# Performance work log

Measured on AMD Instinct MI355X. Metric: run time of the kernel, lower is better.

## Reference

```python
import jax, jax.numpy as jnp
import numpy as np

NEG_SLOPE = 0.2


def _gat_layer(x, W, a_src, a_dst, b, src, dst, heads, out_dim, concat):
    # x: [N, F_in]; W: [F_in, heads*out_dim]; a_src/a_dst: [heads, out_dim]
    N = x.shape[0]
    h = (x @ W).reshape(N, heads, out_dim)              # [N, H, D]
    alpha_src = jnp.sum(h * a_src[None], axis=-1)       # [N, H]
    alpha_dst = jnp.sum(h * a_dst[None], axis=-1)       # [N, H]
    e = jax.nn.leaky_relu(alpha_src[src] + alpha_dst[dst], NEG_SLOPE)  # [E, H]
    # scatter-softmax over incoming edges of each destination node
    e_max = jax.ops.segment_max(e, dst, num_segments=N)            # [N, H]
    e_exp = jnp.exp(e - e_max[dst])                                 # [E, H]
    e_sum = jax.ops.segment_sum(e_exp, dst, num_segments=N)        # [N, H]
    alpha = e_exp / e_sum[dst]                                      # [E, H]
    # weighted scatter-sum of source features
    msg = alpha[:, :, None] * h[src]                                # [E, H, D]
    out = jax.ops.segment_sum(msg, dst, num_segments=N)             # [N, H, D]
    if concat:
        out = out.reshape(N, heads * out_dim)
    else:
        out = out.mean(axis=1)
    return out + b


def setup_inputs() -> dict:
    key = jax.random.key(0)
    ks = jax.random.split(key, 9)
    N, E, F_in, C = 100000, 1600000, 512, 40
    x = jax.random.normal(ks[0], (N, F_in), dtype=jnp.float32)
    edge_index = jax.random.randint(ks[1], (2, E), 0, N, dtype=jnp.int64)
    s = 0.05
    return {
        "x": x,
        "edge_index": edge_index,
        "W1": jax.random.normal(ks[2], (F_in, 64), dtype=jnp.float32) * s,
        "att_src1": jax.random.normal(ks[3], (8, 8), dtype=jnp.float32) * s,
        "att_dst1": jax.random.normal(ks[4], (8, 8), dtype=jnp.float32) * s,
        "b1": jnp.zeros((64,), dtype=jnp.float32),
        "W2": jax.random.normal(ks[5], (64, C), dtype=jnp.float32) * s,
        "att_src2": jax.random.normal(ks[6], (1, C), dtype=jnp.float32) * s,
        "att_dst2": jax.random.normal(ks[7], (1, C), dtype=jnp.float32) * s,
        "b2": jnp.zeros((C,), dtype=jnp.float32),
    }


def reference(x, edge_index, W1, att_src1, att_dst1, b1, W2, att_src2, att_dst2, b2):
    N = x.shape[0]
    # PyG GATConv default add_self_loops=True
    loops = jnp.tile(jnp.arange(N, dtype=edge_index.dtype)[None, :], (2, 1))
    ei = jnp.concatenate([edge_index, loops], axis=1)
    src, dst = ei[0], ei[1]
    # dropout layers are identity at inference
    h = _gat_layer(x, W1, att_src1, att_dst1, b1, src, dst, heads=8, out_dim=8, concat=True)
    h = jax.nn.elu(h)
    out = _gat_layer(h, W2, att_src2, att_dst2, b2, src, dst, heads=1, out_dim=40, concat=True)
    return jax.nn.log_softmax(out, axis=1)
```

## Files before the change

### kernel.cpp

```cpp
#include <hip/hip_runtime.h>
#include <hip/hip_bf16.h>

typedef __bf16 bf16x8 __attribute__((ext_vector_type(8)));
typedef float f32x4 __attribute__((ext_vector_type(4)));
typedef unsigned u32x2 __attribute__((ext_vector_type(2)));
typedef unsigned u32x4 __attribute__((ext_vector_type(4)));

#define LR_SLOPE 0.2f
#define NBKMAX 256
#define BCAP   12288

static __device__ __forceinline__ unsigned short f2bf(float f){
  union { float f; unsigned u; } v; v.f = f;
  unsigned u = v.u;
  u += 0x7fffu + ((u >> 16) & 1u);
  return (unsigned short)(u >> 16);
}
static __device__ __forceinline__ float bf2f(unsigned short us){
  union { unsigned u; float f; } v; v.u = ((unsigned)us) << 16;
  return v.f;
}
static __device__ __forceinline__ unsigned pk2(float a, float b){
  return (unsigned)f2bf(a) | ((unsigned)f2bf(b) << 16);
}
static __device__ __forceinline__ unsigned char f2e4m3(float f){
  return (unsigned char)(__builtin_amdgcn_cvt_pk_fp8_f32(f, 0.f, 0, false) & 0xff);
}
static __device__ __forceinline__ float e4m32f(unsigned b){
  return __builtin_amdgcn_cvt_f32_fp8(b, 0);
}
typedef float f32x4v __attribute__((ext_vector_type(4)));
static __device__ __forceinline__ f32x4v ntl4(const float* p){
  return __builtin_nontemporal_load((const f32x4v*)p);
}

__global__ void prep_w_kernel(const float* __restrict__ W1, const float* __restrict__ W2,
                              unsigned short* __restrict__ wt1, unsigned short* __restrict__ wt2,
                              int* __restrict__ bcnt){
  int t = blockIdx.x*256 + threadIdx.x;
  if (t < 512*64){
    int k = t >> 6, n = t & 63;
    wt1[n*512 + k] = f2bf(W1[t]);
  } else if (t < 512*64 + 48*64){
    int t2 = t - 512*64;
    int c = t2 >> 6, k = t2 & 63;
    wt2[t2] = (c < 40) ? f2bf(W2[k*40 + c]) : (unsigned short)0;
  } else {
    int t3 = t - (512*64 + 48*64);
    if (t3 < NBKMAX) bcnt[t3] = 0;
  }
}

__global__ __launch_bounds__(256) void gemm1_kernel(
    const float* __restrict__ x, const unsigned short* __restrict__ wt1,
    const float* __restrict__ aw_s, const float* __restrict__ aw_d,
    unsigned char* __restrict__ h1p,
    unsigned short* __restrict__ as1p, float* __restrict__ ad1, int N)
{
  __shared__ unsigned short Alds[64*72];
  const int tid = threadIdx.x;
  const int wv = tid >> 6, lane = tid & 63;
  const int c0 = lane & 15, g = lane >> 4;
  const int rowbase = blockIdx.x * 64;

  const int sr = tid >> 2, sq = tid & 3;
  const int grow = rowbase + sr;
  const bool rv = grow < N;
  const float* xp = x + (size_t)grow*512 + sq*16;
  unsigned short* wls = Alds + sr*72 + sq*16;

  f32x4 acc[4];
  acc[0] = acc[1] = acc[2] = acc[3] = (f32x4){0.f,0.f,0.f,0.f};

  const unsigned short* bp0 = wt1 + (size_t)(wv*16 + c0)*512 + g*8;

  for (int kt = 0; kt < 8; ++kt){
    f32x4v f0 = {0,0,0,0}, f1 = {0,0,0,0}, f2 = {0,0,0,0}, f3 = {0,0,0,0};
    if (rv){
      const float* p = xp + kt*64;
      f0 = ntl4(p); f1 = ntl4(p+4); f2 = ntl4(p+8); f3 = ntl4(p+12);
    }
    u32x4 w0 = { pk2(f0.x,f0.y), pk2(f0.z,f0.w), pk2(f1.x,f1.y), pk2(f1.z,f1.w) };
    u32x4 w1 = { pk2(f2.x,f2.y), pk2(f2.z,f2.w), pk2(f3.x,f3.y), pk2(f3.z,f3.w) };
    if (kt) __syncthreads();
    *(u32x4*)wls       = w0;
    *(u32x4*)(wls + 8) = w1;
    __syncthreads();
    bf16x8 b0 = *(const bf16x8*)(bp0 + kt*64);
    bf16x8 b1 = *(const bf16x8*)(bp0 + kt*64 + 32);
    #pragma unroll
    for (int mi = 0; mi < 4; ++mi){
      const unsigned short* ap = Alds + (mi*16 + c0)*72 + g*8;
      bf16x8 a0 = *(const bf16x8*)ap;
      bf16x8 a1 = *(const bf16x8*)(ap + 32);
      acc[mi] = __builtin_amdgcn_mfma_f32_16x16x32_bf16(a0, b0, acc[mi], 0,0,0);
      acc[mi] = __builtin_amdgcn_mfma_f32_16x16x32_bf16(a1, b1, acc[mi], 0,0,0);
    }
  }
  const int hh = wv*2 + (c0 >> 3);
  const float aws_l = aw_s[hh*8 + (c0 & 7)];
  const float awd_l = aw_d[hh*8 + (c0 & 7)];
  #pragma unroll
  for (int mi = 0; mi < 4; ++mi){
    #pragma unroll
    for (int i = 0; i < 4; ++i){
      int row = rowbase + mi*16 + 4*g + i;
      float av = acc[mi][i];
      if (row < N) h1p[(size_t)row*64 + wv*16 + c0] = f2e4m3(av);
      float ss = av * aws_l;
      float dd = av * awd_l;
      ss += __shfl_xor(ss, 1); ss += __shfl_xor(ss, 2); ss += __shfl_xor(ss, 4);
      dd += __shfl_xor(dd, 1); dd += __shfl_xor(dd, 2); dd += __shfl_xor(dd, 4);
      if (row < N && (c0 & 7) == 0){
        as1p[row*8 + hh] = f2bf(ss);
        ad1[row*8 + hh]  = dd;
      }
    }
  }
}

__global__ __launch_bounds__(256) void bucketA_kernel(
    const int* __restrict__ ei, int* __restrict__ bcnt,
    unsigned* __restrict__ bucketed, int E, int M, int NBK)
{
  __shared__ int hist[NBKMAX];
  __shared__ int gb[NBKMAX];
  const int tid = threadIdx.x;
  const int t0 = blockIdx.x * 2048;
  for (int i = tid; i < NBK; i += 256) hist[i] = 0;
  __syncthreads();

  unsigned pe[8]; int bk[8], rnk[8];
  #pragma unroll
  for (int j = 0; j < 8; ++j){
    int m = t0 + j*256 + tid;
    if (m < M){
      int s, d;
      if (m < E){ s = ei[m]; d = ei[E + m]; }
      else      { s = d = m - E; }
      bk[j] = d >> 9;
      pe[j] = ((unsigned)s << 9) | (unsigned)(d & 511);
      rnk[j] = atomicAdd(&hist[bk[j]], 1);
    } else bk[j] = -1;
  }
  __syncthreads();
  for (int i = tid; i < NBK; i += 256) gb[i] = atomicAdd(&bcnt[i], hist[i]);
  __syncthreads();
  #pragma unroll
  for (int j = 0; j < 8; ++j){
    if (bk[j] >= 0) bucketed[(size_t)bk[j]*BCAP + gb[bk[j]] + rnk[j]] = pe[j];
  }
}

__global__ void scanB_kernel(const int* __restrict__ bcnt, int* __restrict__ bstart,
                             int* __restrict__ rowstart, int NBK, int N, int M){
  __shared__ int sc[256];
  int t = threadIdx.x;
  int v = (t < NBK) ? bcnt[t] : 0;
  sc[t] = v; __syncthreads();
  for (int off = 1; off < 256; off <<= 1){
    int u = (t >= off) ? sc[t-off] : 0;
    __syncthreads();
    sc[t] += u;
    __syncthreads();
  }
  if (t < NBK) bstart[t] = sc[t] - v;
  if (t == 0) rowstart[N] = M;
}

__global__ __launch_bounds__(512) void bucketB_kernel(
    const unsigned* __restrict__ bucketed, const int* __restrict__ bcnt,
    const int* __restrict__ bstart,
    int* __restrict__ rowstart, int* __restrict__ csr, int N)
{
  __shared__ int cnt[512];
  __shared__ int cur[512];
  const int k = blockIdx.x;
  const int nodebase = k << 9;
  const int nn = min(512, N - nodebase);
  const int t = threadIdx.x;
  cnt[t] = 0;
  __syncthreads();
  const int ck = bcnt[k];
  const unsigned* bp = bucketed + (size_t)k*BCAP;
  for (int m = t; m < ck; m += 512) atomicAdd(&cnt[bp[m] & 511], 1);
  __syncthreads();
  int myc = cnt[t];
  cur[t] = myc; __syncthreads();
  for (int off = 1; off < 512; off <<= 1){
    int u = (t >= off) ? cur[t-off] : 0;
    __syncthreads();
    cur[t] += u;
    __syncthreads();
  }
  const int base = bstart[k];
  int excl = base + cur[t] - myc;
  if (t < nn) rowstart[nodebase + t] = excl;
  cnt[t] = excl;
  __syncthreads();
  for (int m = t; m < ck; m += 512){
    unsigned e = bp[m];
    int pos = atomicAdd(&cnt[e & 511], 1);
    csr[pos] = (int)(e >> 9);
  }
}

__global__ __launch_bounds__(256) void l1agg_kernel(
    const int* __restrict__ rowstart, const int* __restrict__ csr,
    const unsigned short* __restrict__ as1p,
    const float* __restrict__ ad1,
    const unsigned char* __restrict__ h1p,
    const float* __restrict__ b1,
    unsigned short* __restrict__ g1b, int N)
{
  int wid = blockIdx.x*4 + (threadIdx.x >> 6);
  if (wid >= N) return;
  const int lane = threadIdx.x & 63;
  const int jq  = lane >> 3;
  const int hq  = lane & 7;
  const int par = lane >> 5;
  const int fp  = lane & 31;
  const int hf  = fp >> 2;
  int r0 = rowstart[wid], r1 = rowstart[wid+1];
  int cnt = r1 - r0;
  int cap = cnt < 64 ? cnt : 64;
  int myidx = csr[r0 + (lane < cap ? lane : cap-1)];
  const float advq = ad1[wid*8 + hq];

  float acc0 = 0.f, acc1 = 0.f, den = 0.f;
  for (int c = 0; c < cap; c += 8){
    int se = __shfl(myidx, c + jq);
    float t = bf2f(as1p[se*8 + hq]) + advq;
    t = (t > 0.f) ? t : LR_SLOPE*t;
    float w = __expf(t);
    if (c + jq >= cap) w = 0.f;
    den += w;
    #pragma unroll
    for (int j = 0; j < 4; ++j){
      int s8 = 2*j + par;
      int sj = __shfl(myidx, c + s8);
      float wj = __shfl(w, s8*8 + hf);
      unsigned hv = *(const unsigned short*)(h1p + (size_t)sj*64 + 2*fp);
      acc0 = fmaf(wj, __builtin_amdgcn_cvt_f32_fp8(hv, 0), acc0);
      acc1 = fmaf(wj, __builtin_amdgcn_cvt_f32_fp8(hv, 1), acc1);
    }
  }
  for (int r = r0 + 64; r < r1; ++r){
    int sx = csr[r];
    float t = bf2f(as1p[sx*8 + hq]) + advq;
    t = (t > 0.f) ? t : LR_SLOPE*t;
    float w = __expf(t);
    if (lane < 8) den += w;
    float wj = __shfl(w, hf);
    if (par == 0){
      unsigned hv = *(const unsigned short*)(h1p + (size_t)sx*64 + 2*fp);
      acc0 = fmaf(wj, __builtin_amdgcn_cvt_f32_fp8(hv, 0), acc0);
      acc1 = fmaf(wj, __builtin_amdgcn_cvt_f32_fp8(hv, 1), acc1);
    }
  }
  den += __shfl_xor(den, 8); den += __shfl_xor(den, 16); den += __shfl_xor(den, 32);
  acc0 += __shfl_xor(acc0, 32);
  acc1 += __shfl_xor(acc1, 32);
  if (lane < 32){
    float rdv = 1.f / __shfl(den, hf);
    float v0 = fmaf(acc0, rdv, b1[2*fp]);
    float v1 = fmaf(acc1, rdv, b1[2*fp + 1]);
    v0 = (v0 > 0.f) ? v0 : (__expf(v0) - 1.f);
    v1 = (v1 > 0.f) ? v1 : (__expf(v1) - 1.f);
    ((unsigned*)g1b)[(size_t)wid*32 + fp] = pk2(v0, v1);
  }
}

__global__ __launch_bounds__(256) void gemm2_kernel(
    const unsigned short* __restrict__ g1b, const unsigned short* __restrict__ wt2,
    unsigned char* __restrict__ h2p, int N)
{
  __shared__ unsigned short Alds[64*72];
  const int tid = threadIdx.x;
  const int wv = tid >> 6, lane = tid & 63;
  const int c0 = lane & 15, g = lane >> 4;
  const int rowbase = blockIdx.x * 64;

  const int sr = tid >> 2, sq = tid & 3;
  const int grow = rowbase + sr;
  const bool rv = grow < N;
  u32x4 w0 = {0,0,0,0}, w1 = {0,0,0,0};
  if (rv){
    const u32x4* gp = (const u32x4*)(g1b + (size_t)grow*64 + sq*16);
    w0 = gp[0];
    w1 = gp[1];
  }
  unsigned short* wls = Alds + sr*72 + sq*16;
  *(u32x4*)wls       = w0;
  *(u32x4*)(wls + 8) = w1;
  __syncthreads();

  f32x4 acc[3];
  acc[0] = acc[1] = acc[2] = (f32x4){0.f,0.f,0.f,0.f};
  #pragma unroll
  for (int t2 = 0; t2 < 2; ++t2){
    const unsigned short* ap = Alds + (wv*16 + c0)*72 + t2*32 + g*8;
    bf16x8 a = *(const bf16x8*)ap;
    #pragma unroll
    for (int nf = 0; nf < 3; ++nf){
      bf16x8 b = *(const bf16x8*)(wt2 + (nf*16 + c0)*64 + t2*32 + g*8);
      acc[nf] = __builtin_amdgcn_mfma_f32_16x16x32_bf16(a, b, acc[nf], 0,0,0);
    }
  }
  #pragma unroll
  for (int nf = 0; nf < 3; ++nf){
    int col = nf*16 + c0;
    #pragma unroll
    for (int i = 0; i < 4; ++i){
      int row = rowbase + wv*16 + 4*g + i;
      if (row < N && col < 40) h2p[(size_t)row*40 + col] = f2e4m3(acc[nf][i]);
    }
  }
}

__global__ void attn2_kernel(const unsigned char* __restrict__ h2p,
    const float* __restrict__ aw_s, const float* __restrict__ aw_d,
    float* __restrict__ as2, float* __restrict__ ad2, int N)
{
  int tid = threadIdx.x;
  int wv = blockIdx.x*4 + (tid >> 6);
  int lane = tid & 63;
  int n = wv*8 + (lane >> 3);
  int cq = (lane & 7)*5;
  float s = 0.f, d = 0.f;
  if (n < N){
    const unsigned char* hp = h2p + (size_t)n*40 + cq;
    #pragma unroll
    for (int j = 0; j < 5; ++j){
      float hv = e4m32f(hp[j]);
      s += hv * aw_s[cq + j];
      d += hv * aw_d[cq + j];
    }
  }
  s += __shfl_xor(s, 1); s += __shfl_xor(s, 2); s += __shfl_xor(s, 4);
  d += __shfl_xor(d, 1); d += __shfl_xor(d, 2); d += __shfl_xor(d, 4);
  if (n < N && (lane & 7) == 0){ as2[n] = s; ad2[n] = d; }
}

__global__ __launch_bounds__(256) void l2agg_kernel(
    const int* __restrict__ rowstart, const int* __restrict__ csr,
    const float* __restrict__ as2, const float* __restrict__ ad2,
    const unsigned char* __restrict__ h2p, const float* __restrict__ b2,
    float* __restrict__ out, int N)
{
  int wid = blockIdx.x*4 + (threadIdx.x >> 6);
  if (wid >= N) return;
  const int lane = threadIdx.x & 63;
  const int f = (lane < 40) ? lane : 0;
  int r0 = rowstart[wid], r1 = rowstart[wid+1];
  int cnt = r1 - r0;
  int cap = cnt < 64 ? cnt : 64;
  int myidx = csr[r0 + (lane < cap ? lane : cap-1)];
  const float adv = ad2[wid];

  float t = as2[myidx] + adv;
  t = (t > 0.f) ? t : LR_SLOPE*t;
  float w = __expf(t);
  if (lane >= cap) w = 0.f;
  float den = w;
  #pragma unroll
  for (int off = 32; off; off >>= 1) den += __shfl_xor(den, off);

  float acc = 0.f;
  for (int c = 0; c < cap; c += 4){
    #pragma unroll
    for (int j = 0; j < 4; ++j){
      int slot = c + j;
      int slc  = slot < 63 ? slot : 63;
      float wj = __shfl(w, slc);
      if (slot >= cap) wj = 0.f;
      int sj = __shfl(myidx, slc);
      acc = fmaf(wj, e4m32f(h2p[(size_t)sj*40 + f]), acc);
    }
  }
  for (int r = r0 + 64; r < r1; ++r){
    int sx = csr[r];
    float tt = as2[sx] + adv;
    tt = (tt > 0.f) ? tt : LR_SLOPE*tt;
    float ww = __expf(tt);
    den += ww;
    acc = fmaf(ww, e4m32f(h2p[(size_t)sx*40 + f]), acc);
  }

  float v = (lane < 40) ? (acc/den + b2[f]) : -1e30f;
  float m = v;
  #pragma unroll
  for (int off = 32; off; off >>= 1) m = fmaxf(m, __shfl_xor(m, off));
  float ex = (lane < 40) ? __expf(v - m) : 0.f;
  float sum = ex;
  #pragma unroll
  for (int off = 32; off; off >>= 1) sum += __shfl_xor(sum, off);
  if (lane < 40) out[(size_t)wid*40 + lane] = v - m - __logf(sum);
}

extern "C" void kernel_launch(void* const* d_in, const int* in_sizes, int n_in,
                              void* d_out, int out_size, void* d_ws, size_t ws_size,
                              hipStream_t stream)
{
  const float* x   = (const float*)d_in[0];
  const int*   ei  = (const int*)d_in[1];
  const float* W1  = (const float*)d_in[2];
  const float* aS1 = (const float*)d_in[3];
  const float* aD1 = (const float*)d_in[4];
  const float* b1  = (const float*)d_in[5];
  const float* W2  = (const float*)d_in[6];
  const float* aS2 = (const float*)d_in[7];
  const float* aD2 = (const float*)d_in[8];
  const float* b2  = (const float*)d_in[9];

  const int N   = in_sizes[0] / 512;
  const int E   = in_sizes[1] / 2;
  const int M   = E + N;
  const int NBK = (N + 511) >> 9;

  char* base = (char*)d_ws;
  size_t off = 0;
  auto alloc = [&](size_t bytes)->char* {
    char* p = base + off;
    off += (bytes + 255) & ~(size_t)255;
    return p;
  };
  unsigned char*  h1p  = (unsigned char*)alloc((size_t)N*64);
  unsigned short* g1b  = (unsigned short*)alloc((size_t)N*64*2);
  unsigned short* as1p = (unsigned short*)alloc((size_t)N*8*2);
  float* ad1      = (float*)alloc((size_t)N*8*4);
  int*   rowstart = (int*)alloc((size_t)(N+1)*4);
  int*   bcnt     = (int*)alloc((size_t)NBKMAX*4);
  int*   bstart   = (int*)alloc((size_t)NBKMAX*4);
  int*   csr      = (int*)alloc((size_t)M*4);
  unsigned* bucketed = (unsigned*)alloc((size_t)NBKMAX*BCAP*4);
  unsigned short* wt1 = (unsigned short*)alloc(64*512*2);
  unsigned short* wt2 = (unsigned short*)alloc(48*64*2);
  unsigned char* h2p = h1p;
  float* as2 = (float*)as1p;
  float* ad2 = (float*)ad1;
  float* outp = (float*)d_out;

  prep_w_kernel<<<141, 256, 0, stream>>>(W1, W2, wt1, wt2, bcnt);
  gemm1_kernel<<<(N+63)/64, 256, 0, stream>>>(x, wt1, aS1, aD1, h1p, as1p, ad1, N);
  bucketA_kernel<<<(M+2047)/2048, 256, 0, stream>>>(ei, bcnt, bucketed, E, M, NBK);
  scanB_kernel<<<1, 256, 0, stream>>>(bcnt, bstart, rowstart, NBK, N, M);
  bucketB_kernel<<<NBK, 512, 0, stream>>>(bucketed, bcnt, bstart, rowstart, csr, N);
  l1agg_kernel<<<(N+3)/4, 256, 0, stream>>>(rowstart, csr, as1p, ad1, h1p, b1, g1b, N);
  gemm2_kernel<<<(N+63)/64, 256, 0, stream>>>(g1b, wt2, h2p, N);
  attn2_kernel<<<(N*8+255)/256, 256, 0, stream>>>(h2p, aS2, aD2, as2, ad2, N);
  l2agg_kernel<<<(N+3)/4, 256, 0, stream>>>(rowstart, csr, as2, ad2, h2p, b2, outp, N);
}
```

Measured before the change: 251.7 us.

## Widen gather loads in both aggregations and fuse layer-2 attention into gemm2

The layer-1 aggregation now has each lane read 4 fp8 features (32-bit loads) and covers 4 edges per pass instead of 2, with a wider cross-lane reduction and a vector store of the bf16 output. The layer-2 aggregation regroups the wave into 6 edge groups of 10 lanes, each lane loading 4 fp8 features at once, and combines the groups with shuffles. The log-softmax now uses vector output stores. The separate attn2 kernel is removed: its source/destination attention scores are computed in the gemm2 epilogue from the fp32 accumulators, which saves a launch and a re-read of h2. The scores now come from unquantized values rather than the fp8 copy, and the extra shuffles add some cost.

```diff
diff --git a/kernel.cpp b/kernel.cpp
--- a/kernel.cpp
+++ b/kernel.cpp
@@ -218,16 +218,16 @@
   const int lane = threadIdx.x & 63;
   const int jq  = lane >> 3;
   const int hq  = lane & 7;
-  const int par = lane >> 5;
-  const int fp  = lane & 31;
-  const int hf  = fp >> 2;
+  const int par = lane >> 4;
+  const int q   = lane & 15;
+  const int hh  = q >> 1;
   int r0 = rowstart[wid], r1 = rowstart[wid+1];
   int cnt = r1 - r0;
   int cap = cnt < 64 ? cnt : 64;
   int myidx = csr[r0 + (lane < cap ? lane : cap-1)];
   const float advq = ad1[wid*8 + hq];
 
-  float acc0 = 0.f, acc1 = 0.f, den = 0.f;
+  float a0 = 0.f, a1 = 0.f, a2 = 0.f, a3 = 0.f, den = 0.f;
   for (int c = 0; c < cap; c += 8){
     int se = __shfl(myidx, c + jq);
     float t = bf2f(as1p[se*8 + hq]) + advq;
@@ -236,13 +236,15 @@
     if (c + jq >= cap) w = 0.f;
     den += w;
     #pragma unroll
-    for (int j = 0; j < 4; ++j){
-      int s8 = 2*j + par;
+    for (int j = 0; j < 2; ++j){
+      int s8 = 4*j + par;
       int sj = __shfl(myidx, c + s8);
-      float wj = __shfl(w, s8*8 + hf);
-      unsigned hv = *(const unsigned short*)(h1p + (size_t)sj*64 + 2*fp);
-      acc0 = fmaf(wj, __builtin_amdgcn_cvt_f32_fp8(hv, 0), acc0);
-      acc1 = fmaf(wj, __builtin_amdgcn_cvt_f32_fp8(hv, 1), acc1);
+      float wj = __shfl(w, s8*8 + hh);
+      unsigned hv = *(const unsigned*)(h1p + (size_t)sj*64 + 4*q);
+      a0 = fmaf(wj, __builtin_amdgcn_cvt_f32_fp8(hv, 0), a0);
+      a1 = fmaf(wj, __builtin_amdgcn_cvt_f32_fp8(hv, 1), a1);
+      a2 = fmaf(wj, __builtin_amdgcn_cvt_f32_fp8(hv, 2), a2);
+      a3 = fmaf(wj, __builtin_amdgcn_cvt_f32_fp8(hv, 3), a3);
     }
   }
   for (int r = r0 + 64; r < r1; ++r){
@@ -251,29 +253,39 @@
     t = (t > 0.f) ? t : LR_SLOPE*t;
     float w = __expf(t);
     if (lane < 8) den += w;
-    float wj = __shfl(w, hf);
+    float wj = __shfl(w, hh);
     if (par == 0){
-      unsigned hv = *(const unsigned short*)(h1p + (size_t)sx*64 + 2*fp);
-      acc0 = fmaf(wj, __builtin_amdgcn_cvt_f32_fp8(hv, 0), acc0);
-      acc1 = fmaf(wj, __builtin_amdgcn_cvt_f32_fp8(hv, 1), acc1);
+      unsigned hv = *(const unsigned*)(h1p + (size_t)sx*64 + 4*q);
+      a0 = fmaf(wj, __builtin_amdgcn_cvt_f32_fp8(hv, 0), a0);
+      a1 = fmaf(wj, __builtin_amdgcn_cvt_f32_fp8(hv, 1), a1);
+      a2 = fmaf(wj, __builtin_amdgcn_cvt_f32_fp8(hv, 2), a2);
+      a3 = fmaf(wj, __builtin_amdgcn_cvt_f32_fp8(hv, 3), a3);
     }
   }
   den += __shfl_xor(den, 8); den += __shfl_xor(den, 16); den += __shfl_xor(den, 32);
-  acc0 += __shfl_xor(acc0, 32);
-  acc1 += __shfl_xor(acc1, 32);
-  if (lane < 32){
-    float rdv = 1.f / __shfl(den, hf);
-    float v0 = fmaf(acc0, rdv, b1[2*fp]);
-    float v1 = fmaf(acc1, rdv, b1[2*fp + 1]);
+  a0 += __shfl_xor(a0, 16); a0 += __shfl_xor(a0, 32);
+  a1 += __shfl_xor(a1, 16); a1 += __shfl_xor(a1, 32);
+  a2 += __shfl_xor(a2, 16); a2 += __shfl_xor(a2, 32);
+  a3 += __shfl_xor(a3, 16); a3 += __shfl_xor(a3, 32);
+  if (lane < 16){
+    float rdv = 1.f / __shfl(den, hh);
+    float v0 = fmaf(a0, rdv, b1[4*q]);
+    float v1 = fmaf(a1, rdv, b1[4*q + 1]);
+    float v2 = fmaf(a2, rdv, b1[4*q + 2]);
+    float v3 = fmaf(a3, rdv, b1[4*q + 3]);
     v0 = (v0 > 0.f) ? v0 : (__expf(v0) - 1.f);
     v1 = (v1 > 0.f) ? v1 : (__expf(v1) - 1.f);
-    ((unsigned*)g1b)[(size_t)wid*32 + fp] = pk2(v0, v1);
+    v2 = (v2 > 0.f) ? v2 : (__expf(v2) - 1.f);
+    v3 = (v3 > 0.f) ? v3 : (__expf(v3) - 1.f);
+    u32x2 pk = { pk2(v0, v1), pk2(v2, v3) };
+    *(u32x2*)(g1b + (size_t)wid*64 + 4*q) = pk;
   }
 }
 
 __global__ __launch_bounds__(256) void gemm2_kernel(
     const unsigned short* __restrict__ g1b, const unsigned short* __restrict__ wt2,
-    unsigned char* __restrict__ h2p, int N)
+    const float* __restrict__ aw_s, const float* __restrict__ aw_d,
+    unsigned char* __restrict__ h2p, float* __restrict__ as2, float* __restrict__ ad2, int N)
 {
   __shared__ unsigned short Alds[64*72];
   const int tid = threadIdx.x;
@@ -307,39 +319,30 @@
       acc[nf] = __builtin_amdgcn_mfma_f32_16x16x32_bf16(a, b, acc[nf], 0,0,0);
     }
   }
-  #pragma unroll
-  for (int nf = 0; nf < 3; ++nf){
-    int col = nf*16 + c0;
+  float aws[3], awd[3];
+  aws[0] = aw_s[c0];      awd[0] = aw_d[c0];
+  aws[1] = aw_s[16 + c0]; awd[1] = aw_d[16 + c0];
+  aws[2] = (c0 < 8) ? aw_s[32 + c0] : 0.f;
+  awd[2] = (c0 < 8) ? aw_d[32 + c0] : 0.f;
+  #pragma unroll
+  for (int i = 0; i < 4; ++i){
+    int row = rowbase + wv*16 + 4*g + i;
+    float ss = 0.f, dd = 0.f;
     #pragma unroll
-    for (int i = 0; i < 4; ++i){
-      int row = rowbase + wv*16 + 4*g + i;
-      if (row < N && col < 40) h2p[(size_t)row*40 + col] = f2e4m3(acc[nf][i]);
-    }
-  }
-}
-
-__global__ void attn2_kernel(const unsigned char* __restrict__ h2p,
-    const float* __restrict__ aw_s, const float* __restrict__ aw_d,
-    float* __restrict__ as2, float* __restrict__ ad2, int N)
-{
-  int tid = threadIdx.x;
-  int wv = blockIdx.x*4 + (tid >> 6);
-  int lane = tid & 63;
-  int n = wv*8 + (lane >> 3);
-  int cq = (lane & 7)*5;
-  float s = 0.f, d = 0.f;
-  if (n < N){
-    const unsigned char* hp = h2p + (size_t)n*40 + cq;
-    #pragma unroll
-    for (int j = 0; j < 5; ++j){
-      float hv = e4m32f(hp[j]);
-      s += hv * aw_s[cq + j];
-      d += hv * aw_d[cq + j];
-    }
-  }
-  s += __shfl_xor(s, 1); s += __shfl_xor(s, 2); s += __shfl_xor(s, 4);
-  d += __shfl_xor(d, 1); d += __shfl_xor(d, 2); d += __shfl_xor(d, 4);
-  if (n < N && (lane & 7) == 0){ as2[n] = s; ad2[n] = d; }
+    for (int nf = 0; nf < 3; ++nf){
+      int col = nf*16 + c0;
+      float av = acc[nf][i];
+      if (row < N && col < 40) h2p[(size_t)row*40 + col] = f2e4m3(av);
+      float m = (col < 40) ? av : 0.f;
+      ss = fmaf(m, aws[nf], ss);
+      dd = fmaf(m, awd[nf], dd);
+    }
+    ss += __shfl_xor(ss, 1); ss += __shfl_xor(ss, 2);
+    ss += __shfl_xor(ss, 4); ss += __shfl_xor(ss, 8);
+    dd += __shfl_xor(dd, 1); dd += __shfl_xor(dd, 2);
+    dd += __shfl_xor(dd, 4); dd += __shfl_xor(dd, 8);
+    if (row < N && c0 == 0){ as2[row] = ss; ad2[row] = dd; }
+  }
 }
 
 __global__ __launch_bounds__(256) void l2agg_kernel(
@@ -351,7 +354,9 @@
   int wid = blockIdx.x*4 + (threadIdx.x >> 6);
   if (wid >= N) return;
   const int lane = threadIdx.x & 63;
-  const int f = (lane < 40) ? lane : 0;
+  const int eg = lane / 10;
+  const int ql = lane - eg*10;
+  const bool gl = lane < 60;
   int r0 = rowstart[wid], r1 = rowstart[wid+1];
   int cnt = r1 - r0;
   int cap = cnt < 64 ? cnt : 64;
@@ -366,16 +371,19 @@
   #pragma unroll
   for (int off = 32; off; off >>= 1) den += __shfl_xor(den, off);
 
-  float acc = 0.f;
-  for (int c = 0; c < cap; c += 4){
-    #pragma unroll
-    for (int j = 0; j < 4; ++j){
-      int slot = c + j;
-      int slc  = slot < 63 ? slot : 63;
-      float wj = __shfl(w, slc);
-      if (slot >= cap) wj = 0.f;
-      int sj = __shfl(myidx, slc);
-      acc = fmaf(wj, e4m32f(h2p[(size_t)sj*40 + f]), acc);
+  float a0 = 0.f, a1 = 0.f, a2 = 0.f, a3 = 0.f;
+  for (int c = 0; c < cap; c += 6){
+    int slot = c + eg;
+    int slc  = slot < 63 ? slot : 63;
+    float wj = __shfl(w, slc);
+    if (slot >= cap || !gl) wj = 0.f;
+    int sj = __shfl(myidx, slc);
+    if (gl){
+      unsigned hv = *(const unsigned*)(h2p + (size_t)sj*40 + 4*ql);
+      a0 = fmaf(wj, __builtin_amdgcn_cvt_f32_fp8(hv, 0), a0);
+      a1 = fmaf(wj, __builtin_amdgcn_cvt_f32_fp8(hv, 1), a1);
+      a2 = fmaf(wj, __builtin_amdgcn_cvt_f32_fp8(hv, 2), a2);
+      a3 = fmaf(wj, __builtin_amdgcn_cvt_f32_fp8(hv, 3), a3);
     }
   }
   for (int r = r0 + 64; r < r1; ++r){
@@ -384,18 +392,39 @@
     tt = (tt > 0.f) ? tt : LR_SLOPE*tt;
     float ww = __expf(tt);
     den += ww;
-    acc = fmaf(ww, e4m32f(h2p[(size_t)sx*40 + f]), acc);
-  }
-
-  float v = (lane < 40) ? (acc/den + b2[f]) : -1e30f;
-  float m = v;
+    if (eg == 0){
+      unsigned hv = *(const unsigned*)(h2p + (size_t)sx*40 + 4*ql);
+      a0 = fmaf(ww, __builtin_amdgcn_cvt_f32_fp8(hv, 0), a0);
+      a1 = fmaf(ww, __builtin_amdgcn_cvt_f32_fp8(hv, 1), a1);
+      a2 = fmaf(ww, __builtin_amdgcn_cvt_f32_fp8(hv, 2), a2);
+      a3 = fmaf(ww, __builtin_amdgcn_cvt_f32_fp8(hv, 3), a3);
+    }
+  }
+  float t0 = a0, t1 = a1, t2 = a2, t3 = a3;
+  #pragma unroll
+  for (int gix = 1; gix < 6; ++gix){
+    int src = ((eg + gix) % 6)*10 + ql;
+    t0 += __shfl(a0, src);
+    t1 += __shfl(a1, src);
+    t2 += __shfl(a2, src);
+    t3 += __shfl(a3, src);
+  }
+  float rdv = 1.f/den;
+  float v0 = gl ? fmaf(t0, rdv, b2[4*ql])     : -1e30f;
+  float v1 = gl ? fmaf(t1, rdv, b2[4*ql + 1]) : -1e30f;
+  float v2 = gl ? fmaf(t2, rdv, b2[4*ql + 2]) : -1e30f;
+  float v3 = gl ? fmaf(t3, rdv, b2[4*ql + 3]) : -1e30f;
+  float m = fmaxf(fmaxf(v0, v1), fmaxf(v2, v3));
   #pragma unroll
   for (int off = 32; off; off >>= 1) m = fmaxf(m, __shfl_xor(m, off));
-  float ex = (lane < 40) ? __expf(v - m) : 0.f;
-  float sum = ex;
+  float sum = (eg == 0) ? (__expf(v0-m) + __expf(v1-m) + __expf(v2-m) + __expf(v3-m)) : 0.f;
   #pragma unroll
   for (int off = 32; off; off >>= 1) sum += __shfl_xor(sum, off);
-  if (lane < 40) out[(size_t)wid*40 + lane] = v - m - __logf(sum);
+  if (eg == 0){
+    float ls = m + __logf(sum);
+    f32x4 o = { v0 - ls, v1 - ls, v2 - ls, v3 - ls };
+    *(f32x4*)(out + (size_t)wid*40 + 4*ql) = o;
+  }
 }
 
 extern "C" void kernel_launch(void* const* d_in, const int* in_sizes, int n_in,
@@ -447,7 +476,6 @@
   scanB_kernel<<<1, 256, 0, stream>>>(bcnt, bstart, rowstart, NBK, N, M);
   bucketB_kernel<<<NBK, 512, 0, stream>>>(bucketed, bcnt, bstart, rowstart, csr, N);
   l1agg_kernel<<<(N+3)/4, 256, 0, stream>>>(rowstart, csr, as1p, ad1, h1p, b1, g1b, N);
-  gemm2_kernel<<<(N+63)/64, 256, 0, stream>>>(g1b, wt2, h2p, N);
-  attn2_kernel<<<(N*8+255)/256, 256, 0, stream>>>(h2p, aS2, aD2, as2, ad2, N);
+  gemm2_kernel<<<(N+63)/64, 256, 0, stream>>>(g1b, wt2, aS2, aD2, h2p, as2, ad2, N);
   l2agg_kernel<<<(N+3)/4, 256, 0, stream>>>(rowstart, csr, as2, ad2, h2p, b2, outp, N);
 }
```

After: 253.5 us. No clear change (+0.7%).
